# Kernel tuning notes

Measured on AMD Instinct MI355X. Metric: run time of the kernel, lower is better.

## Reference

```python
import jax, jax.numpy as jnp
import numpy as np

N_HEAD = 16
MASKED_BIAS = -10000.0


def setup_inputs() -> dict:
    key = jax.random.key(0)
    k1, k2, k3 = jax.random.split(key, 3)
    B, S, D = 2, 2048, 1024
    scale_in = 0.02  # GPT-2 style init scale for weights
    return {
        "hidden_states": jax.random.normal(k1, (B, S, D), dtype=jnp.float32),
        "c_attn_w": jax.random.normal(k2, (D, 3 * D), dtype=jnp.float32) * scale_in,
        "c_attn_b": jnp.zeros((3 * D,), dtype=jnp.float32),
        "c_proj_w": jax.random.normal(k3, (D, D), dtype=jnp.float32) * scale_in,
        "c_proj_b": jnp.zeros((D,), dtype=jnp.float32),
    }


def reference(hidden_states, c_attn_w, c_attn_b, c_proj_w, c_proj_b):
    B, S, D = hidden_states.shape
    H = N_HEAD
    hd = D // H

    # Conv1D (HF): x @ W + b, fused QKV
    qkv = hidden_states @ c_attn_w + c_attn_b          # [B, S, 3D]
    q, k, v = jnp.split(qkv, 3, axis=-1)

    def to_heads(x):  # [B, S, D] -> [B, H, S, hd]
        return x.reshape(B, S, H, hd).transpose(0, 2, 1, 3)

    q, k, v = to_heads(q), to_heads(k), to_heads(v)

    # scaled scores (scale=True divides by sqrt(head_dim))
    w = jnp.einsum("bhqd,bhkd->bhqk", q, k) / jnp.float32(hd) ** 0.5  # [B,H,S,S]

    # causal mask via torch.where(mask, w, masked_bias)
    causal = jnp.tril(jnp.ones((S, S), dtype=bool))
    w = jnp.where(causal, w, jnp.float32(MASKED_BIAS))

    w = jax.nn.softmax(w, axis=-1)
    # attn_dropout / resid_dropout are identity in eval mode

    out = jnp.einsum("bhqk,bhkd->bhqd", w, v)          # [B,H,S,hd]
    out = out.transpose(0, 2, 1, 3).reshape(B, S, D)   # merge heads

    return out @ c_proj_w + c_proj_b                   # [B,S,D]
```

## Files before the change

kernel.cpp:

```cpp
#include <hip/hip_runtime.h>
#include <hip/hip_bf16.h>

typedef __attribute__((ext_vector_type(8))) short bf16x8;
typedef __attribute__((ext_vector_type(4))) float f32x4;
typedef __attribute__((ext_vector_type(4))) unsigned u32x4;

#define B_SZ 2
#define S_SZ 2048
#define D_SZ 1024
#define H_SZ 16
#define HD_SZ 64

static __device__ __forceinline__ short f2bf(float f) {
    unsigned u = __builtin_bit_cast(unsigned, f);
    u += 0x7FFFu + ((u >> 16) & 1u);
    return (short)(u >> 16);
}

static __device__ __forceinline__ float fexp2(float x) {
    float r; asm("v_exp_f32 %0, %1" : "=v"(r) : "v"(x)); return r;
}

static __device__ __forceinline__ unsigned cvtpk(float lo, float hi) {
    unsigned r; asm("v_cvt_pk_bf16_f32 %0, %1, %2" : "=v"(r) : "v"(lo), "v"(hi)); return r;
}

static __device__ __forceinline__ void gload16(const short* g, short* l) {
    __builtin_amdgcn_global_load_lds(
        (const __attribute__((address_space(1))) unsigned*)g,
        (__attribute__((address_space(3))) unsigned*)l,
        16, 0, 0);
}

#define SBAR() do { __builtin_amdgcn_sched_barrier(0); \
                    __builtin_amdgcn_s_barrier(); \
                    __builtin_amdgcn_sched_barrier(0); } while (0)

__global__ __launch_bounds__(256) void k_prep(const float* __restrict__ hs, short* __restrict__ Xb,
                                              const float* __restrict__ w1, short* __restrict__ W1T,
                                              const float* __restrict__ w2, short* __restrict__ W2T) {
    __shared__ float tile[32][33];
    const int id = blockIdx.x;
    const int tid = threadIdx.x;
    if (id < 4096) {
        int i = (id * 256 + tid) * 4;
        float4 v = *reinterpret_cast<const float4*>(hs + i);
        short4 o;
        o.x = f2bf(v.x); o.y = f2bf(v.y); o.z = f2bf(v.z); o.w = f2bf(v.w);
        *reinterpret_cast<short4*>(Xb + i) = o;
        return;
    }
    const float* in;
    short* out;
    int N, bx, by;
    if (id < 7168) {
        int bid = id - 4096;
        in = w1; out = W1T; N = 3072;
        bx = bid % 96; by = bid / 96;
    } else {
        int bid = id - 7168;
        in = w2; out = W2T; N = 1024;
        bx = bid & 31; by = bid >> 5;
    }
    const int k0 = by * 32, n0 = bx * 32;
    const int tx = tid & 31, ty = tid >> 5;
    #pragma unroll
    for (int i = 0; i < 4; ++i)
        tile[ty + i * 8][tx] = in[(size_t)(k0 + ty + i * 8) * N + n0 + tx];
    __syncthreads();
    #pragma unroll
    for (int i = 0; i < 4; ++i)
        out[(size_t)(n0 + ty + i * 8) * 1024 + k0 + tx] = f2bf(tile[tx][ty + i * 8]);
}

__global__ __launch_bounds__(512, 1) void k_gemm_qkv8(
    const short* __restrict__ A, const short* __restrict__ Bt,
    const float* __restrict__ bias,
    short* __restrict__ Qo, short* __restrict__ Ko, short* __restrict__ VTo) {
    constexpr int K = 1024, NT = 16;
    __shared__ short As[2][256 * 64];
    __shared__ short Bs[2][192 * 64];
    const int tid = threadIdx.x;
    const int lane = tid & 63;
    const int w = tid >> 6;
    const int wr = w >> 2, wc = w & 3;
    const int lr = lane & 15, lc = lane >> 4;
    const int bid = blockIdx.x;
    const int xcd = bid & 7, local = bid >> 3;
    const int bm = (xcd >> 1) * 4 + (local >> 3);
    const int bn = (xcd & 1) * 8 + (local & 7);
    const size_t arow0 = (size_t)bm * 256;
    const size_t brow0 = (size_t)bn * 192;

    const int srl = tid >> 3;
    const int sc8 = (tid & 7) ^ (srl & 7);
    const int dcol = (tid & 7) * 8;

    f32x4 acc[8][3];
    #pragma unroll
    for (int m = 0; m < 8; ++m)
        #pragma unroll
        for (int n = 0; n < 3; ++n)
            acc[m][n] = (f32x4){0.f, 0.f, 0.f, 0.f};

    auto STAGE_A = [&](int T) {
        const int buf = T & 1;
        #pragma unroll
        for (int j = 0; j < 4; ++j) {
            int row = j * 64 + srl;
            gload16(&A[(arow0 + row) * K + T * 64 + sc8 * 8], &As[buf][row * 64 + dcol]);
        }
    };
    auto STAGE_B = [&](int T) {
        const int buf = T & 1;
        #pragma unroll
        for (int j = 0; j < 3; ++j) {
            int row = j * 64 + srl;
            gload16(&Bt[(brow0 + row) * K + T * 64 + sc8 * 8], &Bs[buf][row * 64 + dcol]);
        }
    };

    const int rx = (lr & 7) * 8;
    auto LDA = [&](int buf, int rowoff, int c) {
        return *reinterpret_cast<const bf16x8*>(
            &As[buf][(wr * 128 + rowoff + lr) * 64 + (((c * 32) + lc * 8) ^ rx)]);
    };
    auto LDB = [&](int buf, int n, int c) {
        return *reinterpret_cast<const bf16x8*>(
            &Bs[buf][(wc * 48 + n * 16 + lr) * 64 + (((c * 32) + lc * 8) ^ rx)]);
    };

    bf16x8 at[4][2];
    bf16x8 bfr[3][2];

    STAGE_A(0); STAGE_B(0); STAGE_B(1);
    asm volatile("s_waitcnt vmcnt(3)" ::: "memory");
    SBAR();

    for (int T = 0; T < NT; ++T) {
        const int buf = T & 1;
        #pragma unroll
        for (int m = 0; m < 4; ++m)
            #pragma unroll
            for (int c = 0; c < 2; ++c)
                at[m][c] = LDA(buf, m * 16, c);
        #pragma unroll
        for (int n = 0; n < 3; ++n)
            #pragma unroll
            for (int c = 0; c < 2; ++c)
                bfr[n][c] = LDB(buf, n, c);
        if (T + 1 < NT) STAGE_A(T + 1);
        SBAR();
        __builtin_amdgcn_s_setprio(1);
        #pragma unroll
        for (int m = 0; m < 4; ++m)
            #pragma unroll
            for (int n = 0; n < 3; ++n)
                #pragma unroll
                for (int c = 0; c < 2; ++c)
                    acc[m][n] = __builtin_amdgcn_mfma_f32_16x16x32_bf16(at[m][c], bfr[n][c], acc[m][n], 0, 0, 0);
        __builtin_amdgcn_s_setprio(0);
        SBAR();
        #pragma unroll
        for (int m = 0; m < 4; ++m)
            #pragma unroll
            for (int c = 0; c < 2; ++c)
                at[m][c] = LDA(buf, 64 + m * 16, c);
        if (T + 2 < NT) {
            STAGE_B(T + 2);
            asm volatile("s_waitcnt vmcnt(3)" ::: "memory");
        } else {
            asm volatile("s_waitcnt vmcnt(0)" ::: "memory");
        }
        SBAR();
        __builtin_amdgcn_s_setprio(1);
        #pragma unroll
        for (int m = 0; m < 4; ++m)
            #pragma unroll
            for (int n = 0; n < 3; ++n)
                #pragma unroll
                for (int c = 0; c < 2; ++c)
                    acc[4 + m][n] = __builtin_amdgcn_mfma_f32_16x16x32_bf16(at[m][c], bfr[n][c], acc[4 + m][n], 0, 0, 0);
        __builtin_amdgcn_s_setprio(0);
        SBAR();
    }

    #pragma unroll
    for (int n = 0; n < 3; ++n) {
        const int col = bn * 192 + wc * 48 + n * 16 + lr;
        const float bv = bias[col];
        if (col < 2048) {
            const bool isq = (col < 1024);
            const float scale = isq ? 0.18033688011112042f : 1.0f;
            short* dst = isq ? Qo : Ko;
            const int dg = col & 1023;
            const int hh = dg >> 6, dd = dg & 63;
            #pragma unroll
            for (int m = 0; m < 8; ++m) {
                #pragma unroll
                for (int r = 0; r < 4; ++r) {
                    int grow = bm * 256 + wr * 128 + m * 16 + lc * 4 + r;
                    int b = grow >> 11, s = grow & 2047;
                    dst[(((size_t)(b * H_SZ + hh)) * S_SZ + s) * HD_SZ + dd] = f2bf((acc[m][n][r] + bv) * scale);
                }
            }
        } else {
            const int dv = col - 2048;
            const int hh = dv >> 6, dt = dv & 63;
            #pragma unroll
            for (int m = 0; m < 8; ++m) {
                int grow = bm * 256 + wr * 128 + m * 16 + lc * 4;
                int b = grow >> 11, s = grow & 2047;
                short4 st;
                st.x = f2bf(acc[m][n][0] + bv);
                st.y = f2bf(acc[m][n][1] + bv);
                st.z = f2bf(acc[m][n][2] + bv);
                st.w = f2bf(acc[m][n][3] + bv);
                *reinterpret_cast<short4*>(
                    &VTo[(((size_t)(b * H_SZ + hh)) * HD_SZ + dt) * S_SZ + s]) = st;
            }
        }
    }
}

__global__ __launch_bounds__(256) void k_attn(const short* __restrict__ Q,
                                              const short* __restrict__ Kv,
                                              const short* __restrict__ VT,
                                              short* __restrict__ O) {
    __shared__ short Ks[3][64 * 64];
    __shared__ short Vs[3][64 * 64];
    const int id = blockIdx.x;
    const int bh = ((id & 7) << 2) | ((id >> 3) & 3);
    const int h = bh & 15;
    const int bb = bh >> 4;
    const int g = id >> 5, oct = g >> 3, gr = g & 7;
    const int qt = (oct == 0) ? 31 - gr : (oct == 1) ? 16 + gr : (oct == 2) ? 15 - gr : gr;
    const int tid = threadIdx.x;
    const int lane = tid & 63, w = tid >> 6;
    const int lr = lane & 15, lc = lane >> 4;
    const int qrow0 = qt * 64 + w * 16;
    const size_t base = (size_t)bh * S_SZ * HD_SZ;

    bf16x8 qf[2];
    #pragma unroll
    for (int c = 0; c < 2; ++c)
        qf[c] = *reinterpret_cast<const bf16x8*>(&Q[base + (size_t)(qrow0 + lr) * HD_SZ + c * 32 + lc * 8]);

    float l_run = 0.f;
    f32x4 o_acc[4];
    #pragma unroll
    for (int n = 0; n < 4; ++n) o_acc[n] = (f32x4){0.f, 0.f, 0.f, 0.f};

    const int srow = tid >> 3;
    const int sslot = (tid & 7) ^ (srow & 7);
    const short* kp = &Kv[base + (size_t)srow * HD_SZ + sslot * 8];
    const short* vp = &VT[base + (size_t)srow * S_SZ + sslot * 8];
    auto STAGE = [&](int b) {
        gload16(kp, &Ks[b][tid * 8]);
        gload16(kp + 2048, &Ks[b][2048 + tid * 8]);
        gload16(vp, &Vs[b][tid * 8]);
        gload16(vp + 32 * S_SZ, &Vs[b][2048 + tid * 8]);
        kp += 4096; vp += 64;
    };

    const int q_row = qrow0 + lr;
    const int rxa = (lr & 7) * 8;
    const bool b0 = (lane & 16) != 0;
    const bool b1 = (lane & 32) != 0;

    STAGE(0);
    if (qt >= 1) {
        STAGE(1);
        asm volatile("s_waitcnt vmcnt(4)" ::: "memory");
    } else {
        asm volatile("s_waitcnt vmcnt(0)" ::: "memory");
    }
    SBAR();

    int bufc = 0, stc = 2;
    for (int kt = 0; kt <= qt; ++kt) {
        if (kt + 2 <= qt) STAGE(stc);
        {
            f32x4 sf[4];
            #pragma unroll
            for (int n = 0; n < 4; ++n) {
                f32x4 z = (f32x4){0.f, 0.f, 0.f, 0.f};
                #pragma unroll
                for (int c = 0; c < 2; ++c) {
                    bf16x8 kf = *reinterpret_cast<const bf16x8*>(
                        &Ks[bufc][(n * 16 + lr) * 64 + ((c * 32 + lc * 8) ^ rxa)]);
                    z = __builtin_amdgcn_mfma_f32_16x16x32_bf16(kf, qf[c], z, 0, 0, 0);
                }
                sf[n] = z;
            }
            if (kt == qt) {
                const int kb = kt * 64 + lc * 4 - q_row;
                #pragma unroll
                for (int n = 0; n < 4; ++n)
                    #pragma unroll
                    for (int r = 0; r < 4; ++r)
                        sf[n][r] = (kb + n * 16 + r > 0) ? -14427.0f : sf[n][r];
            }
            float rs = 0.f;
            #pragma unroll
            for (int n = 0; n < 4; ++n)
                #pragma unroll
                for (int r = 0; r < 4; ++r) {
                    float pv = fexp2(sf[n][r]);
                    sf[n][r] = pv;
                    rs += pv;
                }
            l_run += rs;
            unsigned Apk0 = cvtpk(sf[0][0], sf[0][1]), Apk1 = cvtpk(sf[0][2], sf[0][3]);
            unsigned Bpk0 = cvtpk(sf[1][0], sf[1][1]), Bpk1 = cvtpk(sf[1][2], sf[1][3]);
            unsigned Cpk0 = cvtpk(sf[2][0], sf[2][1]), Cpk1 = cvtpk(sf[2][2], sf[2][3]);
            unsigned Dpk0 = cvtpk(sf[3][0], sf[3][1]), Dpk1 = cvtpk(sf[3][2], sf[3][3]);
            unsigned x0 = __shfl_xor(b0 ? Apk0 : Bpk0, 16);
            unsigned x1 = __shfl_xor(b0 ? Apk1 : Bpk1, 16);
            unsigned x2 = __shfl_xor(b0 ? Cpk0 : Dpk0, 16);
            unsigned x3 = __shfl_xor(b0 ? Cpk1 : Dpk1, 16);
            unsigned y0 = __shfl_xor(b1 ? Apk0 : Bpk0, 32);
            unsigned y1 = __shfl_xor(b1 ? Apk1 : Bpk1, 32);
            unsigned y2 = __shfl_xor(b1 ? Cpk0 : Dpk0, 32);
            unsigned y3 = __shfl_xor(b1 ? Cpk1 : Dpk1, 32);
            unsigned z0 = __shfl_xor(b1 ? Apk0 : Bpk0, 48);
            unsigned z1 = __shfl_xor(b1 ? Apk1 : Bpk1, 48);
            unsigned z2 = __shfl_xor(b1 ? Cpk0 : Dpk0, 48);
            unsigned z3 = __shfl_xor(b1 ? Cpk1 : Dpk1, 48);
            u32x4 pv0 = { b1 ? (b0 ? x0 : y0) : (b0 ? z0 : Apk0),
                          b1 ? (b0 ? x1 : y1) : (b0 ? z1 : Apk1),
                          b1 ? (b0 ? Bpk0 : z0) : (b0 ? y0 : x0),
                          b1 ? (b0 ? Bpk1 : z1) : (b0 ? y1 : x1) };
            u32x4 pv1 = { b1 ? (b0 ? x2 : y2) : (b0 ? z2 : Cpk0),
                          b1 ? (b0 ? x3 : y3) : (b0 ? z3 : Cpk1),
                          b1 ? (b0 ? Dpk0 : z2) : (b0 ? y2 : x2),
                          b1 ? (b0 ? Dpk1 : z3) : (b0 ? y3 : x3) };
            bf16x8 paA = __builtin_bit_cast(bf16x8, pv0);
            bf16x8 paB = __builtin_bit_cast(bf16x8, pv1);
            #pragma unroll
            for (int c = 0; c < 2; ++c) {
                bf16x8 pa = c ? paB : paA;
                #pragma unroll
                for (int n = 0; n < 4; ++n) {
                    bf16x8 vf = *reinterpret_cast<const bf16x8*>(
                        &Vs[bufc][(n * 16 + lr) * 64 + ((c * 32 + lc * 8) ^ rxa)]);
                    o_acc[n] = __builtin_amdgcn_mfma_f32_16x16x32_bf16(pa, vf, o_acc[n], 0, 0, 0);
                }
            }
        }
        if (kt < qt) {
            if (kt + 2 <= qt) asm volatile("s_waitcnt vmcnt(4)" ::: "memory");
            else              asm volatile("s_waitcnt vmcnt(0)" ::: "memory");
            SBAR();
        }
        bufc = (bufc == 2) ? 0 : bufc + 1;
        stc  = (stc == 2) ? 0 : stc + 1;
    }

    l_run += __shfl_xor(l_run, 16);
    l_run += __shfl_xor(l_run, 32);
    float li[4];
    #pragma unroll
    for (int r = 0; r < 4; ++r)
        li[r] = 1.0f / __shfl(l_run, lc * 4 + r);
    #pragma unroll
    for (int n = 0; n < 4; ++n) {
        #pragma unroll
        for (int r = 0; r < 4; ++r) {
            float v = o_acc[n][r] * li[r];
            int s = qrow0 + lc * 4 + r;
            O[((size_t)bb * S_SZ + s) * D_SZ + h * 64 + n * 16 + lr] = f2bf(v);
        }
    }
}

__global__ __launch_bounds__(256, 2) void k_gemm_proj(
    const short* __restrict__ A, const short* __restrict__ Bt,
    const float* __restrict__ bias, float* __restrict__ out) {
    constexpr int K = 1024, NT = 16, N = 1024;
    __shared__ short As[2][128 * 64];
    __shared__ short Bs[2][128 * 64];
    const int tid = threadIdx.x;
    const int lane = tid & 63;
    const int w = tid >> 6;
    const int wr = w >> 1, wc = w & 1;
    const int lr = lane & 15, lc = lane >> 4;
    const int bid = blockIdx.x;
    const int xcd = bid & 7, local = bid >> 3;
    const int bm = xcd * 4 + (local & 3);
    const int bn = local >> 2;
    const size_t arow0 = (size_t)bm * 128;
    const size_t brow0 = (size_t)bn * 128;

    const int srl = tid >> 3;
    const int sc8 = (tid & 7) ^ (srl & 7);
    const int dcol = (tid & 7) * 8;

    f32x4 acc[4][4];
    #pragma unroll
    for (int m = 0; m < 4; ++m)
        #pragma unroll
        for (int n = 0; n < 4; ++n)
            acc[m][n] = (f32x4){0.f, 0.f, 0.f, 0.f};

    auto STAGE_A = [&](int T) {
        const int buf = T & 1;
        #pragma unroll
        for (int j = 0; j < 4; ++j) {
            int row = j * 32 + srl;
            gload16(&A[(arow0 + row) * K + T * 64 + sc8 * 8], &As[buf][row * 64 + dcol]);
        }
    };
    auto STAGE_B = [&](int T) {
        const int buf = T & 1;
        #pragma unroll
        for (int j = 0; j < 4; ++j) {
            int row = j * 32 + srl;
            gload16(&Bt[(brow0 + row) * K + T * 64 + sc8 * 8], &Bs[buf][row * 64 + dcol]);
        }
    };

    const int rx = (lr & 7) * 8;
    auto LDA = [&](int buf, int rowoff, int c) {
        return *reinterpret_cast<const bf16x8*>(
            &As[buf][(wr * 64 + rowoff + lr) * 64 + (((c * 32) + lc * 8) ^ rx)]);
    };
    auto LDB = [&](int buf, int n, int c) {
        return *reinterpret_cast<const bf16x8*>(
            &Bs[buf][(wc * 64 + n * 16 + lr) * 64 + (((c * 32) + lc * 8) ^ rx)]);
    };

    bf16x8 at[2][2];
    bf16x8 bfr[4][2];

    STAGE_A(0); STAGE_B(0); STAGE_B(1);
    asm volatile("s_waitcnt vmcnt(4)" ::: "memory");
    SBAR();

    for (int T = 0; T < NT; ++T) {
        const int buf = T & 1;
        #pragma unroll
        for (int m = 0; m < 2; ++m)
            #pragma unroll
            for (int c = 0; c < 2; ++c)
                at[m][c] = LDA(buf, m * 16, c);
        #pragma unroll
        for (int n = 0; n < 4; ++n)
            #pragma unroll
            for (int c = 0; c < 2; ++c)
                bfr[n][c] = LDB(buf, n, c);
        if (T + 1 < NT) STAGE_A(T + 1);
        SBAR();
        __builtin_amdgcn_s_setprio(1);
        #pragma unroll
        for (int m = 0; m < 2; ++m)
            #pragma unroll
            for (int n = 0; n < 4; ++n)
                #pragma unroll
                for (int c = 0; c < 2; ++c)
                    acc[m][n] = __builtin_amdgcn_mfma_f32_16x16x32_bf16(at[m][c], bfr[n][c], acc[m][n], 0, 0, 0);
        __builtin_amdgcn_s_setprio(0);
        SBAR();
        #pragma unroll
        for (int m = 0; m < 2; ++m)
            #pragma unroll
            for (int c = 0; c < 2; ++c)
                at[m][c] = LDA(buf, 32 + m * 16, c);
        if (T + 2 < NT) {
            STAGE_B(T + 2);
            asm volatile("s_waitcnt vmcnt(4)" ::: "memory");
        } else {
            asm volatile("s_waitcnt vmcnt(0)" ::: "memory");
        }
        SBAR();
        __builtin_amdgcn_s_setprio(1);
        #pragma unroll
        for (int m = 0; m < 2; ++m)
            #pragma unroll
            for (int n = 0; n < 4; ++n)
                #pragma unroll
                for (int c = 0; c < 2; ++c)
                    acc[2 + m][n] = __builtin_amdgcn_mfma_f32_16x16x32_bf16(at[m][c], bfr[n][c], acc[2 + m][n], 0, 0, 0);
        __builtin_amdgcn_s_setprio(0);
        SBAR();
    }

    #pragma unroll
    for (int n = 0; n < 4; ++n) {
        const int col = bn * 128 + wc * 64 + n * 16 + lr;
        const float bv = bias[col];
        #pragma unroll
        for (int m = 0; m < 4; ++m) {
            #pragma unroll
            for (int r = 0; r < 4; ++r) {
                int grow = bm * 128 + wr * 64 + m * 16 + lc * 4 + r;
                out[(size_t)grow * N + col] = acc[m][n][r] + bv;
            }
        }
    }
}

extern "C" void kernel_launch(void* const* d_in, const int* in_sizes, int n_in,
                              void* d_out, int out_size, void* d_ws, size_t ws_size,
                              hipStream_t stream) {
    (void)in_sizes; (void)n_in; (void)out_size; (void)ws_size;
    const float* hs     = (const float*)d_in[0];
    const float* w_attn = (const float*)d_in[1];
    const float* b_attn = (const float*)d_in[2];
    const float* w_proj = (const float*)d_in[3];
    const float* b_proj = (const float*)d_in[4];
    float* out = (float*)d_out;
    char* ws = (char*)d_ws;

    short* Xb  = (short*)(ws + 0);
    short* W1T = (short*)(ws + 8388608);
    short* W2T = (short*)(ws + 14680064);
    short* Qb  = (short*)(ws + 16777216);
    short* Kb  = (short*)(ws + 25165824);
    short* VTb = (short*)(ws + 33554432);
    short* Ob  = (short*)(ws + 0);

    k_prep<<<dim3(8192), dim3(256), 0, stream>>>(hs, Xb, w_attn, W1T, w_proj, W2T);
    k_gemm_qkv8<<<dim3(256), dim3(512), 0, stream>>>(Xb, W1T, b_attn, Qb, Kb, VTb);
    k_attn<<<dim3(1024), dim3(256), 0, stream>>>(Qb, Kb, VTb, Ob);
    k_gemm_proj<<<dim3(256), dim3(256), 0, stream>>>(Ob, W2T, b_proj, out);
}
```

Baseline: 97.62 us.

## Use 16x16x16 MFMA for PV to drop cross-lane P shuffles

In the attention kernel, the P·V product now uses the 16x16x16 bf16 MFMA with transposed operands (V as A, P as B). This lets each lane feed its own packed probabilities directly, which removes the twelve cross-lane shuffles and selects that rebuilt the P fragment. The output accumulator layout changes, so the normalization and store are rewritten as vectorized 4-element row stores. s_setprio hints are also placed around the MFMA sections. The trade-off is twice as many, smaller MFMA instructions and 8-byte LDS reads of V.

```diff
diff --git a/kernel.cpp b/kernel.cpp
--- a/kernel.cpp
+++ b/kernel.cpp
@@ -2,14 +2,22 @@
 #include <hip/hip_bf16.h>
 
 typedef __attribute__((ext_vector_type(8))) short bf16x8;
+typedef __attribute__((ext_vector_type(4))) short bf16x4;
 typedef __attribute__((ext_vector_type(4))) float f32x4;
 typedef __attribute__((ext_vector_type(4))) unsigned u32x4;
+typedef __attribute__((ext_vector_type(2))) unsigned u32x2;
 
 #define B_SZ 2
 #define S_SZ 2048
 #define D_SZ 1024
 #define H_SZ 16
 #define HD_SZ 64
+
+#if __has_builtin(__builtin_amdgcn_mfma_f32_16x16x16bf16_1k)
+#define HAVE_MFMA16 1
+#else
+#define HAVE_MFMA16 0
+#endif
 
 static __device__ __forceinline__ short f2bf(float f) {
     unsigned u = __builtin_bit_cast(unsigned, f);
@@ -265,8 +273,10 @@
 
     const int q_row = qrow0 + lr;
     const int rxa = (lr & 7) * 8;
+#if !HAVE_MFMA16
     const bool b0 = (lane & 16) != 0;
     const bool b1 = (lane & 32) != 0;
+#endif
 
     STAGE(0);
     if (qt >= 1) {
@@ -282,6 +292,7 @@
         if (kt + 2 <= qt) STAGE(stc);
         {
             f32x4 sf[4];
+            __builtin_amdgcn_s_setprio(1);
             #pragma unroll
             for (int n = 0; n < 4; ++n) {
                 f32x4 z = (f32x4){0.f, 0.f, 0.f, 0.f};
@@ -293,6 +304,7 @@
                 }
                 sf[n] = z;
             }
+            __builtin_amdgcn_s_setprio(0);
             if (kt == qt) {
                 const int kb = kt * 64 + lc * 4 - q_row;
                 #pragma unroll
@@ -311,6 +323,21 @@
                     rs += pv;
                 }
             l_run += rs;
+#if HAVE_MFMA16
+            __builtin_amdgcn_s_setprio(1);
+            #pragma unroll
+            for (int n = 0; n < 4; ++n) {
+                u32x2 pw = { cvtpk(sf[n][0], sf[n][1]), cvtpk(sf[n][2], sf[n][3]) };
+                bf16x4 pb = __builtin_bit_cast(bf16x4, pw);
+                #pragma unroll
+                for (int m = 0; m < 4; ++m) {
+                    int addr = (16 * m + lr) * 64 + ((2 * n + (lc >> 1)) ^ (lr & 7)) * 8 + 4 * (lc & 1);
+                    bf16x4 vf = *reinterpret_cast<const bf16x4*>(&Vs[bufc][addr]);
+                    o_acc[m] = __builtin_amdgcn_mfma_f32_16x16x16bf16_1k(vf, pb, o_acc[m], 0, 0, 0);
+                }
+            }
+            __builtin_amdgcn_s_setprio(0);
+#else
             unsigned Apk0 = cvtpk(sf[0][0], sf[0][1]), Apk1 = cvtpk(sf[0][2], sf[0][3]);
             unsigned Bpk0 = cvtpk(sf[1][0], sf[1][1]), Bpk1 = cvtpk(sf[1][2], sf[1][3]);
             unsigned Cpk0 = cvtpk(sf[2][0], sf[2][1]), Cpk1 = cvtpk(sf[2][2], sf[2][3]);
@@ -347,6 +374,7 @@
                     o_acc[n] = __builtin_amdgcn_mfma_f32_16x16x32_bf16(pa, vf, o_acc[n], 0, 0, 0);
                 }
             }
+#endif
         }
         if (kt < qt) {
             if (kt + 2 <= qt) asm volatile("s_waitcnt vmcnt(4)" ::: "memory");
@@ -359,6 +387,19 @@
 
     l_run += __shfl_xor(l_run, 16);
     l_run += __shfl_xor(l_run, 32);
+#if HAVE_MFMA16
+    const float li = 1.0f / l_run;
+    #pragma unroll
+    for (int m = 0; m < 4; ++m) {
+        short4 st;
+        st.x = f2bf(o_acc[m][0] * li);
+        st.y = f2bf(o_acc[m][1] * li);
+        st.z = f2bf(o_acc[m][2] * li);
+        st.w = f2bf(o_acc[m][3] * li);
+        *reinterpret_cast<short4*>(
+            &O[((size_t)bb * S_SZ + qrow0 + lr) * D_SZ + h * 64 + 16 * m + 4 * lc]) = st;
+    }
+#else
     float li[4];
     #pragma unroll
     for (int r = 0; r < 4; ++r)
@@ -372,6 +413,7 @@
             O[((size_t)bb * S_SZ + s) * D_SZ + h * 64 + n * 16 + lr] = f2bf(v);
         }
     }
+#endif
 }
 
 __global__ __launch_bounds__(256, 2) void k_gemm_proj(
```

After: 99.38 us. About the same (+1.8%).
